# Kernel tuning notes

Hardware: AMD Instinct MI355X
Metric: run time of the kernel (lower is better)

The kernel has to match this reference:

```python
import jax, jax.numpy as jnp
import numpy as np
from jax import lax

B, T, N, CIN, CH, COUT, K, KS, E = 2, 16, 2048, 32, 64, 64, 3, 3, 32768


def setup_inputs() -> dict:
    key = jax.random.key(0)
    ks = jax.random.split(key, 20)
    s = 0.05
    p = lambda k, shp: s * jax.random.normal(k, shp, dtype=jnp.float32)
    return {
        "X": jax.random.normal(ks[0], (B, T, N, CIN), dtype=jnp.float32),
        "edge_index": jax.random.randint(ks[1], (2, E), 0, N),
        "edge_weight": jax.random.uniform(ks[2], (E,), dtype=jnp.float32),
        "tc1_w1": p(ks[3], (CH, CIN, 1, KS)), "tc1_b1": p(ks[4], (CH,)),
        "tc1_w2": p(ks[5], (CH, CIN, 1, KS)), "tc1_b2": p(ks[6], (CH,)),
        "tc1_w3": p(ks[7], (CH, CIN, 1, KS)), "tc1_b3": p(ks[8], (CH,)),
        "cheb_w": p(ks[9], (K, CH, CH)), "cheb_b": p(ks[10], (CH,)),
        "tc2_w1": p(ks[11], (COUT, CH, 1, KS)), "tc2_b1": p(ks[12], (COUT,)),
        "tc2_w2": p(ks[13], (COUT, CH, 1, KS)), "tc2_b2": p(ks[14], (COUT,)),
        "tc2_w3": p(ks[15], (COUT, CH, 1, KS)), "tc2_b3": p(ks[16], (COUT,)),
        "bn_gamma": jnp.ones((N,), jnp.float32),
        "bn_beta": jnp.zeros((N,), jnp.float32),
    }


def _tconv(X, w1, b1, w2, b2, w3, b3):
    # X: (B, T, N, C) -> (B, C, N, T), gated temporal conv over last axis
    x = jnp.transpose(X, (0, 3, 2, 1))
    dn = ("NCHW", "OIHW", "NCHW")
    c = lambda w, b: lax.conv_general_dilated(x, w, (1, 1), "VALID", dimension_numbers=dn) + b[None, :, None, None]
    out = jax.nn.relu(c(w1, b1) + jax.nn.sigmoid(c(w2, b2)) + c(w3, b3))
    return jnp.transpose(out, (0, 3, 2, 1))


def _cheb(x, edge_index, edge_weight, W, b):
    # ChebConv, sym normalization, lambda_max=2 -> L_hat = -D^{-1/2} A D^{-1/2}
    row, col = edge_index[0], edge_index[1]
    w = jnp.where(row == col, 0.0, edge_weight)  # get_laplacian removes self-loops
    deg = jax.ops.segment_sum(w, row, num_segments=N)
    safe = jnp.where(deg > 0, deg, 1.0)
    dis = jnp.where(deg > 0, lax.rsqrt(safe), 0.0)
    norm = -dis[row] * w * dis[col]  # (E,)

    def prop(z):  # z: (B, T, N, C)
        zm = jnp.moveaxis(z, 2, 0)                      # (N, B, T, C)
        msg = zm[col] * norm[:, None, None, None]       # (E, B, T, C)
        agg = jax.ops.segment_sum(msg, row, num_segments=N)
        return jnp.moveaxis(agg, 0, 2)

    Tx0 = x
    out = jnp.einsum("btnc,co->btno", Tx0, W[0])
    Tx1 = prop(Tx0)
    out = out + jnp.einsum("btnc,co->btno", Tx1, W[1])
    for k in range(2, K):
        Tx2 = 2.0 * prop(Tx1) - Tx0
        out = out + jnp.einsum("btnc,co->btno", Tx2, W[k])
        Tx0, Tx1 = Tx1, Tx2
    return out + b


def reference(X, edge_index, edge_weight, tc1_w1, tc1_b1, tc1_w2, tc1_b2, tc1_w3, tc1_b3,
              cheb_w, cheb_b, tc2_w1, tc2_b1, tc2_w2, tc2_b2, tc2_w3, tc2_b3,
              bn_gamma, bn_beta):
    t1 = _tconv(X, tc1_w1, tc1_b1, tc1_w2, tc1_b2, tc1_w3, tc1_b3)   # (B, T-2, N, CH)
    t2 = jax.nn.relu(_cheb(t1, edge_index, edge_weight, cheb_w, cheb_b))
    t3 = _tconv(t2, tc2_w1, tc2_b1, tc2_w2, tc2_b2, tc2_w3, tc2_b3)  # (B, T-4, N, COUT)
    t = jnp.transpose(t3, (0, 2, 1, 3))  # (B, N, T', COUT): N is BN channel axis
    mu = jnp.mean(t, axis=(0, 2, 3), keepdims=True)
    var = jnp.var(t, axis=(0, 2, 3), keepdims=True)
    t = (t - mu) * lax.rsqrt(var + 1e-5) * bn_gamma[None, :, None, None] + bn_beta[None, :, None, None]
    return jnp.transpose(t, (0, 2, 1, 3))
```

## Files before the change

### kernel.cpp

```cpp
#include <hip/hip_runtime.h>
#include <cstdint>
#include <cstddef>

typedef unsigned short ushort_t;
typedef short bf16x8 __attribute__((ext_vector_type(8)));
typedef unsigned short u16x8 __attribute__((ext_vector_type(8)));
typedef float f32x4 __attribute__((ext_vector_type(4)));

#define N_NODES 2048
#define E_EDGES 32768

constexpr int SMALL_TOTAL = 72128;
constexpr int OFS_T1B1 = 6144;
constexpr int OFS_T1B2 = 12352;
constexpr int OFS_T1B3 = 18560;
constexpr int OFS_CHB  = 30912;
constexpr int OFS_T2B1 = 43264;
constexpr int OFS_T2B2 = 55616;
constexpr int OFS_T2B3 = 67968;
constexpr int OFS_GAM  = 68032;
constexpr int OFS_BET  = 70080;

__device__ __align__(16) ushort_t g_t1b [3670016];
__device__ __align__(16) ushort_t g_tx1b[3670016];
__device__ __align__(16) ushort_t g_tx2b[3670016];
__device__ __align__(16) ushort_t g_t2b [3670016];
__device__ __align__(16) float    g_t3 [3145728];
__device__ float    g_deg[N_NODES];
__device__ int      g_cnt[N_NODES];
__device__ int      g_cur[N_NODES];
__device__ __align__(8) int2 g_csrp[E_EDGES];
__device__ int      g_rowstart[N_NODES + 1];
__device__ __align__(16) ushort_t g_can[SMALL_TOTAL];
__device__ __align__(16) ushort_t g_wb1[18432];
__device__ __align__(16) ushort_t g_wb2[36864];
__device__ __align__(16) ushort_t g_wbc[12288];

__device__ __forceinline__ float bfu(ushort_t u) { return __uint_as_float(((unsigned)u) << 16); }
__device__ __forceinline__ ushort_t f2bf(float f) {
    unsigned u = __float_as_uint(f);
    u = u + 0x7fffu + ((u >> 16) & 1u);
    return (ushort_t)(u >> 16);
}
__device__ __forceinline__ float ldin(const void* p, int i, bool isbf) {
    return isbf ? bfu(((const ushort_t*)p)[i]) : ((const float*)p)[i];
}
#define BF16_ONES_PAIR 0x3F803F80u

struct SmallPtrs { const void* p[16]; };
struct WPtrs { const void* p[7]; };

__global__ void setup_a_kernel(const int* __restrict__ ei, const void* __restrict__ ew,
                               SmallPtrs sp, WPtrs wp, const unsigned* __restrict__ gam) {
    const bool isbf = (gam[0] == BF16_ONES_PAIR);
    int blk = blockIdx.x;
    if (blk < 128) {
        int e = blk * 256 + threadIdx.x;
        int r = ei[e];
        int c = ei[E_EDGES + e];
        float w = (r == c) ? 0.f : ldin(ew, e, isbf);
        atomicAdd(&g_deg[r], w);
        atomicAdd(&g_cnt[r], 1);
        return;
    }
    if (blk < 410) {
        const int sizes[16] = {6144, 64, 6144, 64, 6144, 64, 12288, 64,
                               12288, 64, 12288, 64, 12288, 64, 2048, 2048};
        int idx = (blk - 128) * 256 + threadIdx.x;
        if (idx >= SMALL_TOTAL) return;
        int j = 0, local = idx;
        while (local >= sizes[j]) { local -= sizes[j]; ++j; }
        g_can[idx] = isbf ? ((const ushort_t*)sp.p[j])[local]
                          : f2bf(((const float*)sp.p[j])[local]);
        return;
    }
    int idx = (blk - 410) * 256 + threadIdx.x;
    if (idx < 18432) {
        int j = idx & 7, lane = (idx >> 3) & 63, kk = (idx >> 9) % 3;
        int nt = (idx / 1536) & 3, set = idx / 6144;
        int o = nt * 16 + (lane & 15);
        int k = kk * 32 + (lane >> 4) * 8 + j;
        int ci = k & 31, ks = k >> 5;
        g_wb1[idx] = f2bf(ldin(wp.p[set], o * 96 + ci * 3 + ks, isbf));
    } else if (idx < 18432 + 36864) {
        int t = idx - 18432;
        int j = t & 7, lane = (t >> 3) & 63, kk = (t >> 9) % 6;
        int nt = (t / 3072) & 3, set = t / 12288;
        int o = nt * 16 + (lane & 15);
        int k = kk * 32 + (lane >> 4) * 8 + j;
        int ci = k & 63, ks = k >> 6;
        g_wb2[t] = f2bf(ldin(wp.p[3 + set], o * 192 + ci * 3 + ks, isbf));
    } else {
        int t = idx - 18432 - 36864;
        int j = t & 7, lane = (t >> 3) & 63, kk = (t >> 9) % 6;
        int nt = t / 3072;
        int o = nt * 16 + (lane & 15);
        int k = kk * 32 + (lane >> 4) * 8 + j;
        int sec = k >> 6, c = k & 63;
        g_wbc[t] = f2bf(ldin(wp.p[6], sec * 4096 + c * 64 + o, isbf));
    }
}

__global__ void scan_kernel() {
    __shared__ int part[256];
    __shared__ int pre[256];
    int t = threadIdx.x;
    int base = t * 8;
    int s = 0;
#pragma unroll
    for (int i = 0; i < 8; ++i) s += g_cnt[base + i];
    part[t] = s;
    __syncthreads();
    if (t == 0) {
        int a = 0;
        for (int i = 0; i < 256; ++i) { pre[i] = a; a += part[i]; }
    }
    __syncthreads();
    int a = pre[t];
#pragma unroll
    for (int i = 0; i < 8; ++i) { g_rowstart[base + i] = a; a += g_cnt[base + i]; }
    if (t == 255) g_rowstart[N_NODES] = a;
}

template <int LAYER>
__global__ __launch_bounds__(256) void tconv_mfma_kernel(const void* __restrict__ Xraw,
                                                         const int* __restrict__ ei,
                                                         const void* __restrict__ ew,
                                                         const unsigned* __restrict__ gam) {
    constexpr int CIN_  = (LAYER == 1) ? 32 : 64;
    constexpr int T_in  = (LAYER == 1) ? 16 : 14;
    constexpr int T_out = (LAYER == 1) ? 14 : 12;
    constexpr int KST   = (CIN_ * 3) / 32;
    constexpr int PADK  = (LAYER == 1) ? 104 : 200;
    constexpr int OB1 = (LAYER == 1) ? OFS_T1B1 : OFS_T2B1;
    constexpr int OB2 = (LAYER == 1) ? OFS_T1B2 : OFS_T2B2;
    constexpr int OB3 = (LAYER == 1) ? OFS_T1B3 : OFS_T2B3;

    if constexpr (LAYER == 1) {
        if (blockIdx.x >= 896) {
            bool isbf = (gam[0] == BF16_ONES_PAIR);
            int e = (blockIdx.x - 896) * 256 + threadIdx.x;
            int r = ei[e];
            int c = ei[E_EDGES + e];
            float w = (r == c) ? 0.f : ldin(ew, e, isbf);
            float dr = g_deg[r], dc = g_deg[c];
            float nr = dr > 0.f ? rsqrtf(dr) : 0.f;
            float nc = dc > 0.f ? rsqrtf(dc) : 0.f;
            int pos = atomicAdd(&g_cur[r], 1);
            g_csrp[g_rowstart[r] + pos] = make_int2(c, __float_as_int(-nr * w * nc));
            return;
        }
    }

    __shared__ ushort_t xs[64 * PADK];

    const int tid = threadIdx.x;
    const int lane = tid & 63;
    const int wv = tid >> 6;
    const int m0 = blockIdx.x * 64;
    const int n0 = m0 & (N_NODES - 1);
    const int s  = m0 >> 11;
    const int b  = s / T_out;
    const int t  = s - b * T_out;

#pragma unroll
    for (int ks = 0; ks < 3; ++ks) {
        if constexpr (LAYER == 1) {
            const bool isbf = (gam[0] == BF16_ONES_PAIR);
            const size_t elo = ((size_t)(b * T_in + t + ks) * N_NODES + n0) * 32;
            if (isbf) {
                const ushort4* src = (const ushort4*)((const ushort_t*)Xraw + elo);
                for (int i = tid; i < 512; i += 256) {
                    ushort4 v = src[i];
                    int row = i >> 3, c4 = i & 7;
                    *(ushort4*)&xs[row * PADK + ks * 32 + c4 * 4] = v;
                }
            } else {
                const float4* src = (const float4*)((const float*)Xraw + elo);
                for (int i = tid; i < 512; i += 256) {
                    float4 f = src[i];
                    ushort4 v;
                    v.x = f2bf(f.x); v.y = f2bf(f.y); v.z = f2bf(f.z); v.w = f2bf(f.w);
                    int row = i >> 3, c4 = i & 7;
                    *(ushort4*)&xs[row * PADK + ks * 32 + c4 * 4] = v;
                }
            }
        } else {
            const ushort4* src = (const ushort4*)(g_t2b +
                ((size_t)(b * T_in + t + ks) * N_NODES + n0) * 64);
            for (int i = tid; i < 1024; i += 256) {
                ushort4 v = src[i];
                int row = i >> 4, c4 = i & 15;
                *(ushort4*)&xs[row * PADK + ks * 64 + c4 * 4] = v;
            }
        }
    }
    __syncthreads();

    const ushort_t* WB = (LAYER == 1) ? g_wb1 : g_wb2;
    f32x4 acc[3][4];
#pragma unroll
    for (int st = 0; st < 3; ++st)
#pragma unroll
        for (int nt = 0; nt < 4; ++nt) acc[st][nt] = (f32x4){0.f, 0.f, 0.f, 0.f};

    const int arow = wv * 16 + (lane & 15);
    const int kofs = (lane >> 4) * 8;
#pragma unroll
    for (int kk = 0; kk < KST; ++kk) {
        bf16x8 av = *(const bf16x8*)&xs[arow * PADK + kk * 32 + kofs];
#pragma unroll
        for (int st = 0; st < 3; ++st)
#pragma unroll
            for (int nt = 0; nt < 4; ++nt) {
                bf16x8 bv = ((const bf16x8*)WB)[((st * 4 + nt) * KST + kk) * 64 + lane];
                acc[st][nt] = __builtin_amdgcn_mfma_f32_16x16x32_bf16(av, bv, acc[st][nt], 0, 0, 0);
            }
    }

    const int col = lane & 15;
    const int quad = lane >> 4;
#pragma unroll
    for (int nt = 0; nt < 4; ++nt) {
        int o = nt * 16 + col;
        float b1 = bfu(g_can[OB1 + o]);
        float b2 = bfu(g_can[OB2 + o]);
        float b3 = bfu(g_can[OB3 + o]);
#pragma unroll
        for (int reg = 0; reg < 4; ++reg) {
            int m = m0 + wv * 16 + quad * 4 + reg;
            float q = acc[1][nt][reg] + b2;
            float v = (acc[0][nt][reg] + b1) + 1.f / (1.f + expf(-q)) + (acc[2][nt][reg] + b3);
            v = v > 0.f ? v : 0.f;
            if constexpr (LAYER == 1) g_t1b[(size_t)m * 64 + o] = f2bf(v);
            else                      g_t3 [(size_t)m * 64 + o] = v;
        }
    }
}

template <int MODE>
__global__ __launch_bounds__(256) void prop_kernel() {
    const ushort_t* __restrict__ src = (MODE == 0) ? g_t1b : g_tx1b;
    ushort_t* __restrict__ dst = (MODE == 0) ? g_tx1b : g_tx2b;
    const int n = blockIdx.x;
    const int tid = threadIdx.x;

    if constexpr (MODE == 0) {
        if (blockIdx.x < 8) {
            int z = blockIdx.x * 256 + tid;
            g_deg[z] = 0.f; g_cnt[z] = 0; g_cur[z] = 0;
        }
    }

    const int slice = tid >> 3;
    const int ch8   = (tid & 7) * 8;
    if (slice >= 28) return;

    const int beg = g_rowstart[n], end = g_rowstart[n + 1];
    const size_t soff = (size_t)slice * (N_NODES * 64) + ch8;

    float a[8];
#pragma unroll
    for (int k = 0; k < 8; ++k) a[k] = 0.f;

    int e = beg;
    for (; e + 4 <= end; e += 4) {
        int2 p0 = g_csrp[e];
        int2 p1 = g_csrp[e + 1];
        int2 p2 = g_csrp[e + 2];
        int2 p3 = g_csrp[e + 3];
        float w0 = __int_as_float(p0.y);
        float w1 = __int_as_float(p1.y);
        float w2 = __int_as_float(p2.y);
        float w3 = __int_as_float(p3.y);
        u16x8 v0 = *(const u16x8*)&src[soff + ((size_t)p0.x << 6)];
        u16x8 v1 = *(const u16x8*)&src[soff + ((size_t)p1.x << 6)];
        u16x8 v2 = *(const u16x8*)&src[soff + ((size_t)p2.x << 6)];
        u16x8 v3 = *(const u16x8*)&src[soff + ((size_t)p3.x << 6)];
#pragma unroll
        for (int k = 0; k < 8; ++k)
            a[k] = fmaf(w0, bfu(v0[k]), fmaf(w1, bfu(v1[k]),
                   fmaf(w2, bfu(v2[k]), fmaf(w3, bfu(v3[k]), a[k]))));
    }
    for (; e < end; ++e) {
        int2 p = g_csrp[e];
        float w = __int_as_float(p.y);
        u16x8 v = *(const u16x8*)&src[soff + ((size_t)p.x << 6)];
#pragma unroll
        for (int k = 0; k < 8; ++k) a[k] = fmaf(w, bfu(v[k]), a[k]);
    }

    const size_t o = soff + ((size_t)n << 6);
    u16x8 r;
    if constexpr (MODE == 0) {
#pragma unroll
        for (int k = 0; k < 8; ++k) r[k] = f2bf(a[k]);
    } else {
        u16x8 t0 = *(const u16x8*)&g_t1b[o];
#pragma unroll
        for (int k = 0; k < 8; ++k) r[k] = f2bf(2.f * a[k] - bfu(t0[k]));
    }
    *(u16x8*)&dst[o] = r;
}

__global__ __launch_bounds__(256) void cheb_mfma_kernel() {
    constexpr int PADK = 200;
    __shared__ ushort_t xs[64 * PADK];

    const int tid = threadIdx.x;
    const int lane = tid & 63;
    const int wv = tid >> 6;
    const int m0 = blockIdx.x * 64;

#pragma unroll
    for (int sec = 0; sec < 3; ++sec) {
        const ushort_t* sp = (sec == 0) ? g_t1b : (sec == 1) ? g_tx1b : g_tx2b;
        const ushort4* src = (const ushort4*)(sp + (size_t)m0 * 64);
        for (int i = tid; i < 1024; i += 256) {
            ushort4 v = src[i];
            int row = i >> 4, c4 = i & 15;
            *(ushort4*)&xs[row * PADK + sec * 64 + c4 * 4] = v;
        }
    }
    __syncthreads();

    f32x4 acc[4];
#pragma unroll
    for (int nt = 0; nt < 4; ++nt) acc[nt] = (f32x4){0.f, 0.f, 0.f, 0.f};

    const int arow = wv * 16 + (lane & 15);
    const int kofs = (lane >> 4) * 8;
#pragma unroll
    for (int kk = 0; kk < 6; ++kk) {
        bf16x8 av = *(const bf16x8*)&xs[arow * PADK + kk * 32 + kofs];
#pragma unroll
        for (int nt = 0; nt < 4; ++nt) {
            bf16x8 bv = ((const bf16x8*)g_wbc)[(nt * 6 + kk) * 64 + lane];
            acc[nt] = __builtin_amdgcn_mfma_f32_16x16x32_bf16(av, bv, acc[nt], 0, 0, 0);
        }
    }

    const int col = lane & 15;
    const int quad = lane >> 4;
#pragma unroll
    for (int nt = 0; nt < 4; ++nt) {
        int o = nt * 16 + col;
        float bias = bfu(g_can[OFS_CHB + o]);
#pragma unroll
        for (int reg = 0; reg < 4; ++reg) {
            int m = m0 + wv * 16 + quad * 4 + reg;
            float v = acc[nt][reg] + bias;
            g_t2b[(size_t)m * 64 + o] = f2bf(v > 0.f ? v : 0.f);
        }
    }
}

__global__ __launch_bounds__(256) void bn_fused_kernel(void* __restrict__ outp,
                                                       const unsigned* __restrict__ gam) {
    int n = blockIdx.x;
    int tid = threadIdx.x;
    int q = tid & 15;
    int g = tid >> 4;
    const bool two = (g < 8);

    size_t base0 = ((size_t)(g * N_NODES + n)) * 64 + q * 4;
    float4 v0 = *reinterpret_cast<const float4*>(&g_t3[base0]);
    float s1 = v0.x + v0.y + v0.z + v0.w;
    float s2 = v0.x * v0.x + v0.y * v0.y + v0.z * v0.z + v0.w * v0.w;
    size_t base1 = 0;
    float4 v1 = make_float4(0.f, 0.f, 0.f, 0.f);
    if (two) {
        base1 = ((size_t)((g + 16) * N_NODES + n)) * 64 + q * 4;
        v1 = *reinterpret_cast<const float4*>(&g_t3[base1]);
        s1 += v1.x + v1.y + v1.z + v1.w;
        s2 += v1.x * v1.x + v1.y * v1.y + v1.z * v1.z + v1.w * v1.w;
    }

    __shared__ float r1[256], r2[256];
    __shared__ float sc_s, sh_s;
    r1[tid] = s1;
    r2[tid] = s2;
    __syncthreads();
    for (int st = 128; st > 0; st >>= 1) {
        if (tid < st) { r1[tid] += r1[tid + st]; r2[tid] += r2[tid + st]; }
        __syncthreads();
    }
    if (tid == 0) {
        const float inv = 1.f / 1536.f;
        float mean = r1[0] * inv;
        float var  = r2[0] * inv - mean * mean;
        float rstd = rsqrtf(var + 1e-5f);
        float gm = bfu(g_can[OFS_GAM + n]), be = bfu(g_can[OFS_BET + n]);
        sc_s = rstd * gm;
        sh_s = be - mean * rstd * gm;
    }
    __syncthreads();
    float sc = sc_s, sh = sh_s;
    bool isbf = (gam[0] == BF16_ONES_PAIR);

    if (isbf) {
        ushort4 o0;
        o0.x = f2bf(v0.x * sc + sh); o0.y = f2bf(v0.y * sc + sh);
        o0.z = f2bf(v0.z * sc + sh); o0.w = f2bf(v0.w * sc + sh);
        *reinterpret_cast<ushort4*>((ushort_t*)outp + base0) = o0;
        if (two) {
            ushort4 o1;
            o1.x = f2bf(v1.x * sc + sh); o1.y = f2bf(v1.y * sc + sh);
            o1.z = f2bf(v1.z * sc + sh); o1.w = f2bf(v1.w * sc + sh);
            *reinterpret_cast<ushort4*>((ushort_t*)outp + base1) = o1;
        }
    } else {
        float4 o0 = make_float4(v0.x * sc + sh, v0.y * sc + sh, v0.z * sc + sh, v0.w * sc + sh);
        *reinterpret_cast<float4*>((float*)outp + base0) = o0;
        if (two) {
            float4 o1 = make_float4(v1.x * sc + sh, v1.y * sc + sh, v1.z * sc + sh, v1.w * sc + sh);
            *reinterpret_cast<float4*>((float*)outp + base1) = o1;
        }
    }
}

extern "C" void kernel_launch(void* const* d_in, const int* in_sizes, int n_in,
                              void* d_out, int out_size, void* d_ws, size_t ws_size,
                              hipStream_t stream) {
    const void* X = d_in[0];
    const int* ei = (const int*)d_in[1];
    const void* ew = d_in[2];
    const unsigned* gam = (const unsigned*)d_in[17];

    SmallPtrs sp;
    for (int i = 0; i < 16; ++i) sp.p[i] = d_in[3 + i];
    WPtrs wp;
    wp.p[0] = d_in[3];  wp.p[1] = d_in[5];  wp.p[2] = d_in[7];
    wp.p[3] = d_in[11]; wp.p[4] = d_in[13]; wp.p[5] = d_in[15];
    wp.p[6] = d_in[9];

    setup_a_kernel<<<674, 256, 0, stream>>>(ei, ew, sp, wp, gam);
    scan_kernel<<<1, 256, 0, stream>>>();

    tconv_mfma_kernel<1><<<1024, 256, 0, stream>>>(X, ei, ew, gam);

    prop_kernel<0><<<N_NODES, 256, 0, stream>>>();
    prop_kernel<1><<<N_NODES, 256, 0, stream>>>();
    cheb_mfma_kernel<<<896, 256, 0, stream>>>();

    tconv_mfma_kernel<2><<<768, 256, 0, stream>>>(X, nullptr, nullptr, gam);

    bn_fused_kernel<<<N_NODES, 256, 0, stream>>>(d_out, gam);
}
```

Measured before the change: 177.2 us.

## Fuse scan into setup via last-block pattern and fuse second prop with Cheb MFMA

The single-block scan kernel is folded into the setup kernel: the last block to arrive, detected with an atomic counter, computes the row-start prefix sum. The second Chebyshev propagation is fused with the Chebyshev weight MFMA. Each node block gathers Tx2 for all 28 time slices, stages Tx0/Tx1/Tx2 in LDS and runs the matmul, so the g_tx2b buffer round trip and two launches disappear. In exchange, each block computes only 28 real rows, padded to 32, with scattered stores across slices. The MFMA work is split into 2 m-tiles x 2 n-tiles across the four waves.

```diff
diff --git a/kernel.cpp b/kernel.cpp
--- a/kernel.cpp
+++ b/kernel.cpp
@@ -23,12 +23,12 @@
 
 __device__ __align__(16) ushort_t g_t1b [3670016];
 __device__ __align__(16) ushort_t g_tx1b[3670016];
-__device__ __align__(16) ushort_t g_tx2b[3670016];
 __device__ __align__(16) ushort_t g_t2b [3670016];
 __device__ __align__(16) float    g_t3 [3145728];
 __device__ float    g_deg[N_NODES];
 __device__ int      g_cnt[N_NODES];
 __device__ int      g_cur[N_NODES];
+__device__ int      g_arrive;
 __device__ __align__(8) int2 g_csrp[E_EDGES];
 __device__ int      g_rowstart[N_NODES + 1];
 __device__ __align__(16) ushort_t g_can[SMALL_TOTAL];
@@ -50,76 +50,95 @@
 struct SmallPtrs { const void* p[16]; };
 struct WPtrs { const void* p[7]; };
 
-__global__ void setup_a_kernel(const int* __restrict__ ei, const void* __restrict__ ew,
-                               SmallPtrs sp, WPtrs wp, const unsigned* __restrict__ gam) {
-    const bool isbf = (gam[0] == BF16_ONES_PAIR);
-    int blk = blockIdx.x;
+__device__ __forceinline__ void setup_body(int blk, int tid, const int* __restrict__ ei,
+                                           const void* __restrict__ ew,
+                                           const SmallPtrs& sp, const WPtrs& wp, bool isbf) {
     if (blk < 128) {
-        int e = blk * 256 + threadIdx.x;
+        int e = blk * 256 + tid;
         int r = ei[e];
         int c = ei[E_EDGES + e];
         float w = (r == c) ? 0.f : ldin(ew, e, isbf);
         atomicAdd(&g_deg[r], w);
         atomicAdd(&g_cnt[r], 1);
-        return;
-    }
-    if (blk < 410) {
+    } else if (blk < 410) {
         const int sizes[16] = {6144, 64, 6144, 64, 6144, 64, 12288, 64,
                                12288, 64, 12288, 64, 12288, 64, 2048, 2048};
-        int idx = (blk - 128) * 256 + threadIdx.x;
-        if (idx >= SMALL_TOTAL) return;
-        int j = 0, local = idx;
-        while (local >= sizes[j]) { local -= sizes[j]; ++j; }
-        g_can[idx] = isbf ? ((const ushort_t*)sp.p[j])[local]
-                          : f2bf(((const float*)sp.p[j])[local]);
-        return;
-    }
-    int idx = (blk - 410) * 256 + threadIdx.x;
-    if (idx < 18432) {
-        int j = idx & 7, lane = (idx >> 3) & 63, kk = (idx >> 9) % 3;
-        int nt = (idx / 1536) & 3, set = idx / 6144;
-        int o = nt * 16 + (lane & 15);
-        int k = kk * 32 + (lane >> 4) * 8 + j;
-        int ci = k & 31, ks = k >> 5;
-        g_wb1[idx] = f2bf(ldin(wp.p[set], o * 96 + ci * 3 + ks, isbf));
-    } else if (idx < 18432 + 36864) {
-        int t = idx - 18432;
-        int j = t & 7, lane = (t >> 3) & 63, kk = (t >> 9) % 6;
-        int nt = (t / 3072) & 3, set = t / 12288;
-        int o = nt * 16 + (lane & 15);
-        int k = kk * 32 + (lane >> 4) * 8 + j;
-        int ci = k & 63, ks = k >> 6;
-        g_wb2[t] = f2bf(ldin(wp.p[3 + set], o * 192 + ci * 3 + ks, isbf));
+        int idx = (blk - 128) * 256 + tid;
+        if (idx < SMALL_TOTAL) {
+            int j = 0, local = idx;
+            while (local >= sizes[j]) { local -= sizes[j]; ++j; }
+            g_can[idx] = isbf ? ((const ushort_t*)sp.p[j])[local]
+                              : f2bf(((const float*)sp.p[j])[local]);
+        }
     } else {
-        int t = idx - 18432 - 36864;
-        int j = t & 7, lane = (t >> 3) & 63, kk = (t >> 9) % 6;
-        int nt = t / 3072;
-        int o = nt * 16 + (lane & 15);
-        int k = kk * 32 + (lane >> 4) * 8 + j;
-        int sec = k >> 6, c = k & 63;
-        g_wbc[t] = f2bf(ldin(wp.p[6], sec * 4096 + c * 64 + o, isbf));
-    }
-}
-
-__global__ void scan_kernel() {
+        int idx = (blk - 410) * 256 + tid;
+        if (idx < 18432) {
+            int j = idx & 7, lane = (idx >> 3) & 63, kk = (idx >> 9) % 3;
+            int nt = (idx / 1536) & 3, set = idx / 6144;
+            int o = nt * 16 + (lane & 15);
+            int k = kk * 32 + (lane >> 4) * 8 + j;
+            int ci = k & 31, ks = k >> 5;
+            g_wb1[idx] = f2bf(ldin(wp.p[set], o * 96 + ci * 3 + ks, isbf));
+        } else if (idx < 18432 + 36864) {
+            int t = idx - 18432;
+            int j = t & 7, lane = (t >> 3) & 63, kk = (t >> 9) % 6;
+            int nt = (t / 3072) & 3, set = t / 12288;
+            int o = nt * 16 + (lane & 15);
+            int k = kk * 32 + (lane >> 4) * 8 + j;
+            int ci = k & 63, ks = k >> 6;
+            g_wb2[t] = f2bf(ldin(wp.p[3 + set], o * 192 + ci * 3 + ks, isbf));
+        } else {
+            int t = idx - 18432 - 36864;
+            int j = t & 7, lane = (t >> 3) & 63, kk = (t >> 9) % 6;
+            int nt = t / 3072;
+            int o = nt * 16 + (lane & 15);
+            int k = kk * 32 + (lane >> 4) * 8 + j;
+            int sec = k >> 6, c = k & 63;
+            g_wbc[t] = f2bf(ldin(wp.p[6], sec * 4096 + c * 64 + o, isbf));
+        }
+    }
+}
+
+__global__ __launch_bounds__(256) void setup_scan_kernel(const int* __restrict__ ei,
+                                                         const void* __restrict__ ew,
+                                                         SmallPtrs sp, WPtrs wp,
+                                                         const unsigned* __restrict__ gam) {
+    const bool isbf = (gam[0] == BF16_ONES_PAIR);
+    const int tid = threadIdx.x;
+    setup_body(blockIdx.x, tid, ei, ew, sp, wp, isbf);
+
+    __shared__ bool amlast;
+    __threadfence();
+    if (tid == 0) {
+        int t = __hip_atomic_fetch_add(&g_arrive, 1, __ATOMIC_ACQ_REL,
+                                       __HIP_MEMORY_SCOPE_AGENT);
+        amlast = (t == (int)gridDim.x - 1);
+    }
+    __syncthreads();
+    if (!amlast) return;
+
     __shared__ int part[256];
     __shared__ int pre[256];
-    int t = threadIdx.x;
-    int base = t * 8;
+    int base = tid * 8;
+    int cnt[8];
     int s = 0;
 #pragma unroll
-    for (int i = 0; i < 8; ++i) s += g_cnt[base + i];
-    part[t] = s;
-    __syncthreads();
-    if (t == 0) {
+    for (int i = 0; i < 8; ++i) {
+        cnt[i] = __hip_atomic_load(&g_cnt[base + i], __ATOMIC_RELAXED,
+                                   __HIP_MEMORY_SCOPE_AGENT);
+        s += cnt[i];
+    }
+    part[tid] = s;
+    __syncthreads();
+    if (tid == 0) {
         int a = 0;
         for (int i = 0; i < 256; ++i) { pre[i] = a; a += part[i]; }
     }
     __syncthreads();
-    int a = pre[t];
-#pragma unroll
-    for (int i = 0; i < 8; ++i) { g_rowstart[base + i] = a; a += g_cnt[base + i]; }
-    if (t == 255) g_rowstart[N_NODES] = a;
+    int a = pre[tid];
+#pragma unroll
+    for (int i = 0; i < 8; ++i) { g_rowstart[base + i] = a; a += cnt[i]; }
+    if (tid == 255) g_rowstart[N_NODES] = a;
 }
 
 template <int LAYER>
@@ -127,18 +146,18 @@
                                                          const int* __restrict__ ei,
                                                          const void* __restrict__ ew,
                                                          const unsigned* __restrict__ gam) {
-    constexpr int CIN_  = (LAYER == 1) ? 32 : 64;
     constexpr int T_in  = (LAYER == 1) ? 16 : 14;
     constexpr int T_out = (LAYER == 1) ? 14 : 12;
-    constexpr int KST   = (CIN_ * 3) / 32;
+    constexpr int KST   = (LAYER == 1) ? 3 : 6;
     constexpr int PADK  = (LAYER == 1) ? 104 : 200;
     constexpr int OB1 = (LAYER == 1) ? OFS_T1B1 : OFS_T2B1;
     constexpr int OB2 = (LAYER == 1) ? OFS_T1B2 : OFS_T2B2;
     constexpr int OB3 = (LAYER == 1) ? OFS_T1B3 : OFS_T2B3;
 
+    const bool isbf = (gam[0] == BF16_ONES_PAIR);
+
     if constexpr (LAYER == 1) {
         if (blockIdx.x >= 896) {
-            bool isbf = (gam[0] == BF16_ONES_PAIR);
             int e = (blockIdx.x - 896) * 256 + threadIdx.x;
             int r = ei[e];
             int c = ei[E_EDGES + e];
@@ -152,7 +171,7 @@
         }
     }
 
-    __shared__ ushort_t xs[64 * PADK];
+    __shared__ __align__(16) ushort_t xs[64 * PADK];
 
     const int tid = threadIdx.x;
     const int lane = tid & 63;
@@ -166,7 +185,6 @@
 #pragma unroll
     for (int ks = 0; ks < 3; ++ks) {
         if constexpr (LAYER == 1) {
-            const bool isbf = (gam[0] == BF16_ONES_PAIR);
             const size_t elo = ((size_t)(b * T_in + t + ks) * N_NODES + n0) * 32;
             if (isbf) {
                 const ushort4* src = (const ushort4*)((const ushort_t*)Xraw + elo);
@@ -238,18 +256,15 @@
     }
 }
 
-template <int MODE>
-__global__ __launch_bounds__(256) void prop_kernel() {
-    const ushort_t* __restrict__ src = (MODE == 0) ? g_t1b : g_tx1b;
-    ushort_t* __restrict__ dst = (MODE == 0) ? g_tx1b : g_tx2b;
+__global__ __launch_bounds__(256) void prop0_kernel() {
     const int n = blockIdx.x;
     const int tid = threadIdx.x;
 
-    if constexpr (MODE == 0) {
-        if (blockIdx.x < 8) {
-            int z = blockIdx.x * 256 + tid;
-            g_deg[z] = 0.f; g_cnt[z] = 0; g_cur[z] = 0;
-        }
+    if (blockIdx.x < 8) {
+        int z = blockIdx.x * 256 + tid;
+        g_deg[z] = 0.f; g_cnt[z] = 0; g_cur[z] = 0;
+        if (z == 0) __hip_atomic_store(&g_arrive, 0, __ATOMIC_RELAXED,
+                                       __HIP_MEMORY_SCOPE_AGENT);
     }
 
     const int slice = tid >> 3;
@@ -273,10 +288,10 @@
         float w1 = __int_as_float(p1.y);
         float w2 = __int_as_float(p2.y);
         float w3 = __int_as_float(p3.y);
-        u16x8 v0 = *(const u16x8*)&src[soff + ((size_t)p0.x << 6)];
-        u16x8 v1 = *(const u16x8*)&src[soff + ((size_t)p1.x << 6)];
-        u16x8 v2 = *(const u16x8*)&src[soff + ((size_t)p2.x << 6)];
-        u16x8 v3 = *(const u16x8*)&src[soff + ((size_t)p3.x << 6)];
+        u16x8 v0 = *(const u16x8*)&g_t1b[soff + ((size_t)p0.x << 6)];
+        u16x8 v1 = *(const u16x8*)&g_t1b[soff + ((size_t)p1.x << 6)];
+        u16x8 v2 = *(const u16x8*)&g_t1b[soff + ((size_t)p2.x << 6)];
+        u16x8 v3 = *(const u16x8*)&g_t1b[soff + ((size_t)p3.x << 6)];
 #pragma unroll
         for (int k = 0; k < 8; ++k)
             a[k] = fmaf(w0, bfu(v0[k]), fmaf(w1, bfu(v1[k]),
@@ -285,72 +300,113 @@
     for (; e < end; ++e) {
         int2 p = g_csrp[e];
         float w = __int_as_float(p.y);
-        u16x8 v = *(const u16x8*)&src[soff + ((size_t)p.x << 6)];
+        u16x8 v = *(const u16x8*)&g_t1b[soff + ((size_t)p.x << 6)];
 #pragma unroll
         for (int k = 0; k < 8; ++k) a[k] = fmaf(w, bfu(v[k]), a[k]);
     }
 
     const size_t o = soff + ((size_t)n << 6);
     u16x8 r;
-    if constexpr (MODE == 0) {
-#pragma unroll
-        for (int k = 0; k < 8; ++k) r[k] = f2bf(a[k]);
+#pragma unroll
+    for (int k = 0; k < 8; ++k) r[k] = f2bf(a[k]);
+    *(u16x8*)&g_tx1b[o] = r;
+}
+
+__global__ __launch_bounds__(256) void prop_cheb_kernel() {
+    __shared__ __align__(16) ushort_t xs[32 * 200];
+
+    const int n = blockIdx.x;
+    const int tid = threadIdx.x;
+    const int slice = tid >> 3;
+    const int ch8   = (tid & 7) * 8;
+
+    if (slice < 28) {
+        const int beg = g_rowstart[n], end = g_rowstart[n + 1];
+        const size_t soff = (size_t)slice * (N_NODES * 64) + ch8;
+
+        float a[8];
+#pragma unroll
+        for (int k = 0; k < 8; ++k) a[k] = 0.f;
+
+        int e = beg;
+        for (; e + 4 <= end; e += 4) {
+            int2 p0 = g_csrp[e];
+            int2 p1 = g_csrp[e + 1];
+            int2 p2 = g_csrp[e + 2];
+            int2 p3 = g_csrp[e + 3];
+            float w0 = __int_as_float(p0.y);
+            float w1 = __int_as_float(p1.y);
+            float w2 = __int_as_float(p2.y);
+            float w3 = __int_as_float(p3.y);
+            u16x8 v0 = *(const u16x8*)&g_tx1b[soff + ((size_t)p0.x << 6)];
+            u16x8 v1 = *(const u16x8*)&g_tx1b[soff + ((size_t)p1.x << 6)];
+            u16x8 v2 = *(const u16x8*)&g_tx1b[soff + ((size_t)p2.x << 6)];
+            u16x8 v3 = *(const u16x8*)&g_tx1b[soff + ((size_t)p3.x << 6)];
+#pragma unroll
+            for (int k = 0; k < 8; ++k)
+                a[k] = fmaf(w0, bfu(v0[k]), fmaf(w1, bfu(v1[k]),
+                       fmaf(w2, bfu(v2[k]), fmaf(w3, bfu(v3[k]), a[k]))));
+        }
+        for (; e < end; ++e) {
+            int2 p = g_csrp[e];
+            float w = __int_as_float(p.y);
+            u16x8 v = *(const u16x8*)&g_tx1b[soff + ((size_t)p.x << 6)];
+#pragma unroll
+            for (int k = 0; k < 8; ++k) a[k] = fmaf(w, bfu(v[k]), a[k]);
+        }
+
+        const size_t o = soff + ((size_t)n << 6);
+        u16x8 t0 = *(const u16x8*)&g_t1b[o];
+        u16x8 t1 = *(const u16x8*)&g_tx1b[o];
+        u16x8 t2;
+#pragma unroll
+        for (int k = 0; k < 8; ++k) t2[k] = f2bf(2.f * a[k] - bfu(t0[k]));
+
+        *(u16x8*)&xs[slice * 200 + ch8]        = t0;
+        *(u16x8*)&xs[slice * 200 + 64 + ch8]   = t1;
+        *(u16x8*)&xs[slice * 200 + 128 + ch8]  = t2;
     } else {
-        u16x8 t0 = *(const u16x8*)&g_t1b[o];
-#pragma unroll
-        for (int k = 0; k < 8; ++k) r[k] = f2bf(2.f * a[k] - bfu(t0[k]));
-    }
-    *(u16x8*)&dst[o] = r;
-}
-
-__global__ __launch_bounds__(256) void cheb_mfma_kernel() {
-    constexpr int PADK = 200;
-    __shared__ ushort_t xs[64 * PADK];
-
-    const int tid = threadIdx.x;
+        int r = 28 + ((tid - 224) >> 3);
+        u16x8 z = {0, 0, 0, 0, 0, 0, 0, 0};
+        *(u16x8*)&xs[r * 200 + ch8]       = z;
+        *(u16x8*)&xs[r * 200 + 64 + ch8]  = z;
+        *(u16x8*)&xs[r * 200 + 128 + ch8] = z;
+    }
+    __syncthreads();
+
     const int lane = tid & 63;
     const int wv = tid >> 6;
-    const int m0 = blockIdx.x * 64;
-
-#pragma unroll
-    for (int sec = 0; sec < 3; ++sec) {
-        const ushort_t* sp = (sec == 0) ? g_t1b : (sec == 1) ? g_tx1b : g_tx2b;
-        const ushort4* src = (const ushort4*)(sp + (size_t)m0 * 64);
-        for (int i = tid; i < 1024; i += 256) {
-            ushort4 v = src[i];
-            int row = i >> 4, c4 = i & 15;
-            *(ushort4*)&xs[row * PADK + sec * 64 + c4 * 4] = v;
-        }
-    }
-    __syncthreads();
-
-    f32x4 acc[4];
-#pragma unroll
-    for (int nt = 0; nt < 4; ++nt) acc[nt] = (f32x4){0.f, 0.f, 0.f, 0.f};
-
-    const int arow = wv * 16 + (lane & 15);
+    const int mt = wv >> 1;
+    const int ntb = (wv & 1) * 2;
+    const int arow = mt * 16 + (lane & 15);
     const int kofs = (lane >> 4) * 8;
+
+    f32x4 acc[2];
+    acc[0] = (f32x4){0.f, 0.f, 0.f, 0.f};
+    acc[1] = (f32x4){0.f, 0.f, 0.f, 0.f};
 #pragma unroll
     for (int kk = 0; kk < 6; ++kk) {
-        bf16x8 av = *(const bf16x8*)&xs[arow * PADK + kk * 32 + kofs];
-#pragma unroll
-        for (int nt = 0; nt < 4; ++nt) {
-            bf16x8 bv = ((const bf16x8*)g_wbc)[(nt * 6 + kk) * 64 + lane];
-            acc[nt] = __builtin_amdgcn_mfma_f32_16x16x32_bf16(av, bv, acc[nt], 0, 0, 0);
+        bf16x8 av = *(const bf16x8*)&xs[arow * 200 + kk * 32 + kofs];
+#pragma unroll
+        for (int i = 0; i < 2; ++i) {
+            bf16x8 bv = ((const bf16x8*)g_wbc)[((ntb + i) * 6 + kk) * 64 + lane];
+            acc[i] = __builtin_amdgcn_mfma_f32_16x16x32_bf16(av, bv, acc[i], 0, 0, 0);
         }
     }
 
     const int col = lane & 15;
     const int quad = lane >> 4;
 #pragma unroll
-    for (int nt = 0; nt < 4; ++nt) {
-        int o = nt * 16 + col;
+    for (int i = 0; i < 2; ++i) {
+        int o = (ntb + i) * 16 + col;
         float bias = bfu(g_can[OFS_CHB + o]);
 #pragma unroll
         for (int reg = 0; reg < 4; ++reg) {
-            int m = m0 + wv * 16 + quad * 4 + reg;
-            float v = acc[nt][reg] + bias;
-            g_t2b[(size_t)m * 64 + o] = f2bf(v > 0.f ? v : 0.f);
+            int m = mt * 16 + quad * 4 + reg;
+            if (m < 28) {
+                float v = acc[i][reg] + bias;
+                g_t2b[((size_t)(m * N_NODES + n)) * 64 + o] = f2bf(v > 0.f ? v : 0.f);
+            }
         }
     }
 }
@@ -434,16 +490,10 @@
     wp.p[3] = d_in[11]; wp.p[4] = d_in[13]; wp.p[5] = d_in[15];
     wp.p[6] = d_in[9];
 
-    setup_a_kernel<<<674, 256, 0, stream>>>(ei, ew, sp, wp, gam);
-    scan_kernel<<<1, 256, 0, stream>>>();
-
+    setup_scan_kernel<<<674, 256, 0, stream>>>(ei, ew, sp, wp, gam);
     tconv_mfma_kernel<1><<<1024, 256, 0, stream>>>(X, ei, ew, gam);
-
-    prop_kernel<0><<<N_NODES, 256, 0, stream>>>();
-    prop_kernel<1><<<N_NODES, 256, 0, stream>>>();
-    cheb_mfma_kernel<<<896, 256, 0, stream>>>();
-
+    prop0_kernel<<<N_NODES, 256, 0, stream>>>();
+    prop_cheb_kernel<<<N_NODES, 256, 0, stream>>>();
     tconv_mfma_kernel<2><<<768, 256, 0, stream>>>(X, nullptr, nullptr, gam);
-
     bn_fused_kernel<<<N_NODES, 256, 0, stream>>>(d_out, gam);
 }
```

Result: slower. 219.8 us (+24.1%).
